# Optimization experiments

Measured on AMD Instinct MI355X. Metric: run time of the kernel, lower is better.

Reference implementation:

```python
import jax, jax.numpy as jnp
import numpy as np

N_NODES = 100000
NODES_PER_GRAPH = 100
IN_CHANNELS = 256
RATIO = 0.5


def setup_inputs() -> dict:
    key = jax.random.key(0)
    k_x, k_w, k_b = jax.random.split(key, 3)
    x = jax.random.normal(k_x, (N_NODES, IN_CHANNELS), dtype=jnp.float32)
    # sorted per-node graph ids: 1000 graphs of 100 nodes each
    batch = (jnp.arange(N_NODES, dtype=jnp.int64) // NODES_PER_GRAPH).astype(jnp.int64)
    # Linear(in_channels, 1): weight [1, d], bias [1] (torch default init scale)
    bound = 1.0 / np.sqrt(IN_CHANNELS)
    W = jax.random.uniform(k_w, (1, IN_CHANNELS), dtype=jnp.float32, minval=-bound, maxval=bound)
    b = jax.random.uniform(k_b, (1,), dtype=jnp.float32, minval=-bound, maxval=bound)
    return {"x": x, "batch": batch, "W": W, "b": b}


def reference(x, batch, W, b):
    N = x.shape[0]
    num_graphs = int(batch[-1]) + 1          # static under equal-size segments
    n_per = N // num_graphs
    k = int(np.ceil(RATIO * n_per))          # PyG topk: ceil(ratio * n_i)

    # linear score: [N]
    scores = x @ W[0] + b[0]

    # per-graph segment top-k (segments are equal-size, contiguous)
    grid = scores.reshape(num_graphs, n_per)                  # [G, n_per]
    top_vals, top_idx = jax.lax.top_k(grid, k)                # each [G, k], descending

    offsets = (jnp.arange(num_graphs, dtype=top_idx.dtype) * n_per)[:, None]
    node_index = (top_idx + offsets).reshape(-1)              # [G*k] global node ids
    weight = top_vals.reshape(-1)                             # scores[node_index]
    cluster_index = jnp.arange(node_index.shape[0], dtype=node_index.dtype)
    return node_index, cluster_index, weight
```

## Files before the change

### kernel.cpp

```cpp
#include <hip/hip_runtime.h>
#include <hip/hip_bf16.h>


#define NPG   100
#define DIM   256
#define KSEL  50
#define ROWS_PER_WAVE 25

typedef float vfloat4 __attribute__((ext_vector_type(4)));

static __device__ __forceinline__ float bf2f(unsigned short s) {
    union { unsigned int u; float f; } v;
    v.u = ((unsigned int)s) << 16;
    return v.f;
}

static __device__ __forceinline__ bool probe_f32(const void* xv) {
    const unsigned short* xu = (const unsigned short*)xv;
    bool f32 = false;
    #pragma unroll
    for (int i = 0; i < 64; ++i) {
        const float v = bf2f(xu[2 * i]);
        if (!(v > -64.0f && v < 64.0f)) f32 = true;
    }
    return f32;
}

static __device__ __forceinline__ float mergepair(float a, float b, int lane, int mask) {
    const bool hi = (lane & mask) != 0;
    const float u = hi ? b : a;
    const float w = hi ? a : b;
    return u + __shfl_xor(w, mask, 64);
}

static __device__ __forceinline__ float merge8(const float* p, int lane) {
    float m01 = mergepair(p[0], p[1], lane, 1);
    float m23 = mergepair(p[2], p[3], lane, 1);
    float m45 = mergepair(p[4], p[5], lane, 1);
    float m67 = mergepair(p[6], p[7], lane, 1);
    float m03 = mergepair(m01, m23, lane, 2);
    float m47 = mergepair(m45, m67, lane, 2);
    float m   = mergepair(m03, m47, lane, 4);
    m += __shfl_xor(m, 8, 64);
    m += __shfl_xor(m, 16, 64);
    m += __shfl_xor(m, 32, 64);
    return m;
}

__global__ __launch_bounds__(256) void fused_select_kernel(
    const void* __restrict__ xv,
    const void* __restrict__ Wv,
    const void* __restrict__ bv,
    void* __restrict__ outv,
    int num_graphs)
{
    __shared__ float w_sh[DIM];
    __shared__ float sc[NPG];

    const int tid  = threadIdx.x;
    const int wave = tid >> 6;
    const int lane = tid & 63;
    const int g    = blockIdx.x;

    const bool f32 = probe_f32(xv);

    if (f32) w_sh[tid] = ((const float*)Wv)[tid];
    else     w_sh[tid] = bf2f(((const unsigned short*)Wv)[tid]);
    __syncthreads();

    const float bval = f32 ? ((const float*)bv)[0]
                           : bf2f(((const unsigned short*)bv)[0]);
    const float wl0 = w_sh[lane * 4 + 0];
    const float wl1 = w_sh[lane * 4 + 1];
    const float wl2 = w_sh[lane * 4 + 2];
    const float wl3 = w_sh[lane * 4 + 3];

    const int rbase = wave * ROWS_PER_WAVE;
    const long grow0 = (long)g * NPG + rbase;

    float p[ROWS_PER_WAVE];

    if (f32) {
        const vfloat4* xr = (const vfloat4*)xv;
        vfloat4 u[ROWS_PER_WAVE];
        #pragma unroll
        for (int i = 0; i < ROWS_PER_WAVE; ++i)
            u[i] = __builtin_nontemporal_load(
                       &xr[(size_t)(grow0 + i) * (DIM / 4) + lane]);
        #pragma unroll
        for (int i = 0; i < ROWS_PER_WAVE; ++i)
            p[i] = u[i].x * wl0 + u[i].y * wl1 + u[i].z * wl2 + u[i].w * wl3;
    } else {
        const unsigned short* x = (const unsigned short*)xv;
        ushort4 u[ROWS_PER_WAVE];
        #pragma unroll
        for (int i = 0; i < ROWS_PER_WAVE; ++i)
            u[i] = ((const ushort4*)(x + (size_t)(grow0 + i) * DIM))[lane];
        #pragma unroll
        for (int i = 0; i < ROWS_PER_WAVE; ++i)
            p[i] = bf2f(u[i].x) * wl0 + bf2f(u[i].y) * wl1
                 + bf2f(u[i].z) * wl2 + bf2f(u[i].w) * wl3;
    }

    #pragma unroll
    for (int b = 0; b < 3; ++b) {
        const float m = merge8(&p[b * 8], lane);
        if (lane < 8) sc[rbase + b * 8 + lane] = m + bval;
    }
    {
        float acc = p[24];
        #pragma unroll
        for (int off = 32; off > 0; off >>= 1)
            acc += __shfl_xor(acc, off, 64);
        if (lane == 0) sc[rbase + 24] = acc + bval;
    }
    __syncthreads();

    if (tid < NPG) {
        const float v = sc[tid];
        int rank = 0;
        #pragma unroll 4
        for (int i = 0; i < NPG; ++i) {
            const float vi = sc[i];
            rank += (vi > v) || (vi == v && i < tid);
        }
        if (rank < KSEL) {
            const int total = num_graphs * KSEL;
            const int pos   = g * KSEL + rank;
            const int node  = g * NPG + tid;
            if (f32) {
                float* o = (float*)outv;
                o[pos]             = (float)node;
                o[total + pos]     = (float)pos;
                o[2 * total + pos] = v;
            } else {
                __hip_bfloat16* o = (__hip_bfloat16*)outv;
                o[pos]             = __float2bfloat16((float)node);
                o[total + pos]     = __float2bfloat16((float)pos);
                o[2 * total + pos] = __float2bfloat16(v);
            }
        }
    }
}

extern "C" void kernel_launch(void* const* d_in, const int* in_sizes, int n_in,
                              void* d_out, int out_size, void* d_ws, size_t ws_size,
                              hipStream_t stream) {
    int xi = -1, wi = -1, bi = -1;
    long best = -1;
    for (int i = 0; i < n_in; ++i) {
        const long s = in_sizes[i];
        if (s > best) { best = s; xi = i; }
    }
    for (int i = 0; i < n_in; ++i) {
        if (i == xi) continue;
        const long s = in_sizes[i];
        if (s == DIM && wi < 0) wi = i;
        if (s == 1   && bi < 0) bi = i;
    }
    if (xi < 0) xi = 0;
    if (wi < 0) wi = (n_in > 2) ? 2 : 1;
    if (bi < 0) bi = n_in - 1;

    const long n_rows     = (long)in_sizes[xi] / DIM;
    const long num_graphs = n_rows / NPG;
    if (num_graphs <= 0) return;

    (void)d_ws; (void)ws_size;

    fused_select_kernel<<<dim3((unsigned)num_graphs), dim3(256), 0, stream>>>(
        d_in[xi], d_in[wi], d_in[bi], d_out, (int)num_graphs);
}
```

Measured before the change: 148.8 us.

## Process two graphs per block with software-pipelined row loads

Each block now handles two consecutive graphs. The f32 path is restructured into 8-row chunks whose loads are issued before the dot products and reductions of earlier chunks, so memory latency overlaps compute and register pressure drops. Launch bounds now request 4 blocks per CU, and the top-k ranking for the second graph runs on threads 128+. This halves the grid and amortizes the per-block W load and format probe, at the cost of fewer blocks for load balancing and a longer serial chain per block.

```diff
diff --git a/kernel.cpp b/kernel.cpp
--- a/kernel.cpp
+++ b/kernel.cpp
@@ -47,7 +47,20 @@
     return m;
 }
 
-__global__ __launch_bounds__(256) void fused_select_kernel(
+static __device__ __forceinline__ void load8(vfloat4* u, const vfloat4* base, int row0) {
+    #pragma unroll
+    for (int i = 0; i < 8; ++i)
+        u[i] = __builtin_nontemporal_load(base + (size_t)(row0 + i) * (DIM / 4));
+}
+
+static __device__ __forceinline__ void dot8(float* p, const vfloat4* u,
+                                            float w0, float w1, float w2, float w3) {
+    #pragma unroll
+    for (int i = 0; i < 8; ++i)
+        p[i] = u[i].x * w0 + u[i].y * w1 + u[i].z * w2 + u[i].w * w3;
+}
+
+__global__ __launch_bounds__(256, 4) void fused_select_kernel(
     const void* __restrict__ xv,
     const void* __restrict__ Wv,
     const void* __restrict__ bv,
@@ -55,12 +68,16 @@
     int num_graphs)
 {
     __shared__ float w_sh[DIM];
-    __shared__ float sc[NPG];
+    __shared__ float scA[NPG];
+    __shared__ float scB[NPG];
 
     const int tid  = threadIdx.x;
     const int wave = tid >> 6;
     const int lane = tid & 63;
-    const int g    = blockIdx.x;
+
+    const int gA   = 2 * blockIdx.x;
+    const int gB   = gA + 1;
+    const bool hasB = (gB < num_graphs);
 
     const bool f32 = probe_f32(xv);
 
@@ -76,58 +93,104 @@
     const float wl3 = w_sh[lane * 4 + 3];
 
     const int rbase = wave * ROWS_PER_WAVE;
-    const long grow0 = (long)g * NPG + rbase;
-
-    float p[ROWS_PER_WAVE];
 
     if (f32) {
         const vfloat4* xr = (const vfloat4*)xv;
-        vfloat4 u[ROWS_PER_WAVE];
-        #pragma unroll
-        for (int i = 0; i < ROWS_PER_WAVE; ++i)
-            u[i] = __builtin_nontemporal_load(
-                       &xr[(size_t)(grow0 + i) * (DIM / 4) + lane]);
-        #pragma unroll
-        for (int i = 0; i < ROWS_PER_WAVE; ++i)
-            p[i] = u[i].x * wl0 + u[i].y * wl1 + u[i].z * wl2 + u[i].w * wl3;
+        const vfloat4* bA = xr + (size_t)(gA * NPG + rbase) * (DIM / 4) + lane;
+        const vfloat4* bB = xr + (size_t)((size_t)gB * NPG + rbase) * (DIM / 4) + lane;
+        vfloat4 u0[8], u1[8], uA24, uB24;
+        float p[8];
+
+        load8(u0, bA, 0);
+        load8(u1, bA, 8);
+        dot8(p, u0, wl0, wl1, wl2, wl3);
+        load8(u0, bA, 16);
+        uA24 = __builtin_nontemporal_load(bA + (size_t)24 * (DIM / 4));
+        { const float m = merge8(p, lane); if (lane < 8) scA[rbase + lane] = m + bval; }
+
+        dot8(p, u1, wl0, wl1, wl2, wl3);
+        if (hasB) load8(u1, bB, 0);
+        { const float m = merge8(p, lane); if (lane < 8) scA[rbase + 8 + lane] = m + bval; }
+
+        dot8(p, u0, wl0, wl1, wl2, wl3);
+        if (hasB) load8(u0, bB, 8);
+        { const float m = merge8(p, lane); if (lane < 8) scA[rbase + 16 + lane] = m + bval; }
+
+        {
+            float acc = uA24.x * wl0 + uA24.y * wl1 + uA24.z * wl2 + uA24.w * wl3;
+            #pragma unroll
+            for (int off = 32; off > 0; off >>= 1)
+                acc += __shfl_xor(acc, off, 64);
+            if (lane == 0) scA[rbase + 24] = acc + bval;
+        }
+
+        if (hasB) {
+            dot8(p, u1, wl0, wl1, wl2, wl3);
+            load8(u1, bB, 16);
+            uB24 = __builtin_nontemporal_load(bB + (size_t)24 * (DIM / 4));
+            { const float m = merge8(p, lane); if (lane < 8) scB[rbase + lane] = m + bval; }
+
+            dot8(p, u0, wl0, wl1, wl2, wl3);
+            { const float m = merge8(p, lane); if (lane < 8) scB[rbase + 8 + lane] = m + bval; }
+
+            dot8(p, u1, wl0, wl1, wl2, wl3);
+            { const float m = merge8(p, lane); if (lane < 8) scB[rbase + 16 + lane] = m + bval; }
+
+            {
+                float acc = uB24.x * wl0 + uB24.y * wl1 + uB24.z * wl2 + uB24.w * wl3;
+                #pragma unroll
+                for (int off = 32; off > 0; off >>= 1)
+                    acc += __shfl_xor(acc, off, 64);
+                if (lane == 0) scB[rbase + 24] = acc + bval;
+            }
+        }
     } else {
         const unsigned short* x = (const unsigned short*)xv;
-        ushort4 u[ROWS_PER_WAVE];
-        #pragma unroll
-        for (int i = 0; i < ROWS_PER_WAVE; ++i)
-            u[i] = ((const ushort4*)(x + (size_t)(grow0 + i) * DIM))[lane];
-        #pragma unroll
-        for (int i = 0; i < ROWS_PER_WAVE; ++i)
-            p[i] = bf2f(u[i].x) * wl0 + bf2f(u[i].y) * wl1
-                 + bf2f(u[i].z) * wl2 + bf2f(u[i].w) * wl3;
-    }
-
-    #pragma unroll
-    for (int b = 0; b < 3; ++b) {
-        const float m = merge8(&p[b * 8], lane);
-        if (lane < 8) sc[rbase + b * 8 + lane] = m + bval;
-    }
-    {
-        float acc = p[24];
-        #pragma unroll
-        for (int off = 32; off > 0; off >>= 1)
-            acc += __shfl_xor(acc, off, 64);
-        if (lane == 0) sc[rbase + 24] = acc + bval;
+        for (int gg = 0; gg < (hasB ? 2 : 1); ++gg) {
+            const int g = gA + gg;
+            float* scb = gg ? scB : scA;
+            ushort4 u[ROWS_PER_WAVE];
+            float p[ROWS_PER_WAVE];
+            #pragma unroll
+            for (int i = 0; i < ROWS_PER_WAVE; ++i)
+                u[i] = ((const ushort4*)(x + (size_t)(g * NPG + rbase + i) * DIM))[lane];
+            #pragma unroll
+            for (int i = 0; i < ROWS_PER_WAVE; ++i)
+                p[i] = bf2f(u[i].x) * wl0 + bf2f(u[i].y) * wl1
+                     + bf2f(u[i].z) * wl2 + bf2f(u[i].w) * wl3;
+            #pragma unroll
+            for (int b = 0; b < 3; ++b) {
+                const float m = merge8(&p[b * 8], lane);
+                if (lane < 8) scb[rbase + b * 8 + lane] = m + bval;
+            }
+            {
+                float acc = p[24];
+                #pragma unroll
+                for (int off = 32; off > 0; off >>= 1)
+                    acc += __shfl_xor(acc, off, 64);
+                if (lane == 0) scb[rbase + 24] = acc + bval;
+            }
+        }
     }
     __syncthreads();
 
-    if (tid < NPG) {
-        const float v = sc[tid];
+    const bool doA = (tid < NPG);
+    const bool doB = hasB && (tid >= 128) && (tid < 128 + NPG);
+    if (doA || doB) {
+        const float* sc = doA ? scA : scB;
+        const int    t  = doA ? tid : (tid - 128);
+        const int    g  = doA ? gA  : gB;
+        const float v = sc[t];
         int rank = 0;
         #pragma unroll 4
         for (int i = 0; i < NPG; ++i) {
             const float vi = sc[i];
-            rank += (vi > v) || (vi == v && i < tid);
+            rank += (vi > v) || (vi == v && i < t);
         }
         if (rank < KSEL) {
             const int total = num_graphs * KSEL;
             const int pos   = g * KSEL + rank;
-            const int node  = g * NPG + tid;
+            const int node  = g * NPG + t;
             if (f32) {
                 float* o = (float*)outv;
                 o[pos]             = (float)node;
@@ -168,6 +231,7 @@
 
     (void)d_ws; (void)ws_size;
 
-    fused_select_kernel<<<dim3((unsigned)num_graphs), dim3(256), 0, stream>>>(
+    const unsigned nblocks = (unsigned)((num_graphs + 1) / 2);
+    fused_select_kernel<<<dim3(nblocks), dim3(256), 0, stream>>>(
         d_in[xi], d_in[wi], d_in[bi], d_out, (int)num_graphs);
 }
```

Measured after the change: 145.8 us. 2.0% less time.
